# Optimization experiments

Hardware: AMD Instinct MI355X
Metric: run time of the kernel (lower is better)

Reference implementation:

```python
import jax, jax.numpy as jnp
import numpy as np

B, D, K, NDIM = 4, 81, 2048, 4  # batch, feature dim, n mixture components, box coord dims


def setup_inputs() -> dict:
    key = jax.random.key(0)
    k1, k2, k3, k4 = jax.random.split(key, 4)
    x = jax.random.normal(k1, (B, D, K), dtype=jnp.float32)
    # mixture weights, positive and normalized over components
    pi = jax.nn.softmax(jax.random.normal(k2, (B, 1, K), dtype=jnp.float32), axis=2)
    # component means in [0,1] (normalized box coords)
    mu = jax.random.uniform(k3, (B, NDIM, K), dtype=jnp.float32)
    # positive scales
    sig = jax.random.uniform(k4, (B, NDIM, K), dtype=jnp.float32) * 0.1 + 0.01
    return {"x": x, "pi": pi, "mu": mu, "sig": sig}


def _cauchy_pdf(mu, sig, points):
    # mu, sig: (B, 1, NDIM, K); points: (B, P, NDIM, 1)
    d = points - mu
    return sig / (jnp.pi * (d * d + sig * sig))


def reference(x, pi, mu, sig):
    # points = mu.transpose(1,2): evaluate the mixture at each component mean
    points = jnp.transpose(mu, (0, 2, 1))            # (B, K, NDIM)
    comp = _cauchy_pdf(mu[:, None, :, :], sig[:, None, :, :],
                       points[:, :, :, None])        # (B, K, NDIM, K)
    comp = jnp.prod(comp, axis=2)                    # independent dims -> (B, K, K)
    lh = pi * comp                                   # pi (B,1,K) broadcasts over points
    coef = lh / jnp.sum(lh, axis=2, keepdims=True)   # normalize over components
    coef = jax.lax.stop_gradient(coef)               # coef_detach=True
    y = jnp.einsum('bdk,bkm->bdm', x, coef)          # torch.bmm(x, coef)
    return y
```

## Files before the change

kernel.cpp:

```cpp
#include <hip/hip_runtime.h>


typedef float v4f __attribute__((ext_vector_type(4)));
typedef float f32x4 __attribute__((ext_vector_type(4)));
typedef short bf16x8 __attribute__((ext_vector_type(8)));

namespace {
constexpr int BB = 4;
constexpr int DD = 81;
constexpr int KK = 2048;
constexpr int MROWS = 96;
constexpr float INV_PI4 = 1.0f / 97.40909103400243f;

constexpr size_t OFF_XBF = 0;
constexpr size_t OFF_RSP = (size_t)BB * MROWS * KK * 2;
}

__device__ __forceinline__ unsigned short f2bf(float f) {
    union { float f; unsigned int u; } v; v.f = f;
    unsigned int u = v.u;
    unsigned int r = (u + 0x7FFFu + ((u >> 16) & 1u)) >> 16;
    return (unsigned short)r;
}

__global__ __launch_bounds__(256) void rowsum_kernel(const float* __restrict__ pi_,
                                                     const float* __restrict__ mu,
                                                     const float* __restrict__ sig,
                                                     float* __restrict__ rowsumPart) {
    __shared__ v4f   mush[256];
    __shared__ v4f   s2sh[256];
    __shared__ float csh[256];
    __shared__ float red[4][64];

    int blk = blockIdx.x;
    int b   = blk >> 8;
    int pc  = (blk & 255) >> 3;
    int ms  = blk & 7;
    int p0  = pc * 64;
    int m0  = ms * 256;
    int t   = threadIdx.x;
    int lane = t & 63, w = t >> 6;

    const float* mub = mu  + (size_t)b * 4 * KK;
    const float* sgb = sig + (size_t)b * 4 * KK;
    const float* pib = pi_ + (size_t)b * KK;

    {
        int m = m0 + t;
        v4f mm = {mub[m], mub[KK + m], mub[2 * KK + m], mub[3 * KK + m]};
        v4f sg = {sgb[m], sgb[KK + m], sgb[2 * KK + m], sgb[3 * KK + m]};
        mush[t] = mm;
        s2sh[t] = sg * sg;
        csh[t]  = pib[m] * ((sg.x * sg.y) * (sg.z * sg.w)) * INV_PI4;
    }
    int p = p0 + lane;
    v4f mp = {mub[p], mub[KK + p], mub[2 * KK + p], mub[3 * KK + p]};
    __syncthreads();

    float sum = 0.f;
#pragma unroll 4
    for (int i = 0; i < 64; ++i) {
        int mi = w * 64 + i;
        v4f d = mp - mush[mi];
        v4f q = d * d + s2sh[mi];
        float den = (q.x * q.y) * (q.z * q.w);
        sum += csh[mi] * __builtin_amdgcn_rcpf(den);
    }

    red[w][lane] = sum;
    __syncthreads();
    if (t < 64)
        rowsumPart[((size_t)(b * 8 + ms)) * KK + p0 + t] =
            red[0][t] + red[1][t] + red[2][t] + red[3][t];
}

__global__ __launch_bounds__(256) void xbf_kernel(const float* __restrict__ x,
                                                  const float* __restrict__ rowsumPart,
                                                  unsigned short* __restrict__ xbf) {
    int d = blockIdx.x;
    int b = blockIdx.y;
    int t = threadIdx.x;
    unsigned short* orow = xbf + ((size_t)(b * MROWS + d)) * KK;
    const float* xrow = x + ((size_t)(b * DD + d)) * KK;
    const float* rsp  = rowsumPart + (size_t)b * 8 * KK;
#pragma unroll
    for (int j = 0; j < 8; ++j) {
        int p = j * 256 + t;
        float rs = 0.f;
#pragma unroll
        for (int s = 0; s < 8; ++s) rs += rsp[(size_t)s * KK + p];
        float v = 0.f;
        if (d < DD) v = xrow[p] * __builtin_amdgcn_rcpf(rs);
        orow[p] = f2bf(v);
    }
}

__global__ __launch_bounds__(512) void gemm_kernel(const float* __restrict__ pi_,
                                                   const float* __restrict__ mu,
                                                   const float* __restrict__ sig,
                                                   const unsigned short* __restrict__ xbf,
                                                   float* __restrict__ out) {
    __shared__ __align__(16) char smem[49152];
    v4f* mus = (v4f*)smem;
    f32x4 (*red)[6][64] = (f32x4 (*)[6][64])smem;

    int t = threadIdx.x;
    int w = t >> 6, lane = t & 63;
    int r = lane & 15, q = lane >> 4;
    int b  = blockIdx.y;
    int m0 = blockIdx.x * 16;

    const float* mub = mu  + (size_t)b * 4 * KK;
    const float* sgb = sig + (size_t)b * 4 * KK;

    for (int i = t; i < KK; i += 512)
        mus[i] = (v4f){mub[i], mub[KK + i], mub[2 * KK + i], mub[3 * KK + i]};

    int m = m0 + r;
    v4f mm = {mub[m], mub[KK + m], mub[2 * KK + m], mub[3 * KK + m]};
    v4f sg = {sgb[m], sgb[KK + m], sgb[2 * KK + m], sgb[3 * KK + m]};
    v4f s2 = sg * sg;
    float cm = pi_[(size_t)b * KK + m] * ((sg.x * sg.y) * (sg.z * sg.w)) * INV_PI4;

    const unsigned short* Abase = xbf + ((size_t)(b * MROWS + r)) * KK;

    f32x4 acc[6];
#pragma unroll
    for (int i = 0; i < 6; ++i) acc[i] = (f32x4)0.f;

    __syncthreads();

    int pw = w * 256;
#pragma unroll
    for (int ks = 0; ks < 8; ++ks) {
        int pb = pw + ks * 32 + q * 8;
        bf16x8 Bf;
#pragma unroll
        for (int j = 0; j < 8; ++j) {
            v4f mp = mus[pb + j];
            v4f dd = mp - mm;
            v4f qq = dd * dd + s2;
            float den = (qq.x * qq.y) * (qq.z * qq.w);
            float lh = cm * __builtin_amdgcn_rcpf(den);
            Bf[j] = (short)f2bf(lh);
        }
        bf16x8 Af[6];
#pragma unroll
        for (int Mt = 0; Mt < 6; ++Mt)
            Af[Mt] = *(const bf16x8*)(Abase + (size_t)Mt * 16 * KK + pb);
#pragma unroll
        for (int Mt = 0; Mt < 6; ++Mt)
            acc[Mt] = __builtin_amdgcn_mfma_f32_16x16x32_bf16(Af[Mt], Bf, acc[Mt], 0, 0, 0);
    }

    __syncthreads();
#pragma unroll
    for (int Mt = 0; Mt < 6; ++Mt)
        red[w][Mt][lane] = acc[Mt];
    __syncthreads();

    int col = t & 15;
    int dr  = t >> 4;
#pragma unroll
    for (int k = 0; k < 3; ++k) {
        int d = dr + 32 * k;
        if (d < DD) {
            int Mt  = d >> 4;
            int row = d & 15;
            int l   = (row >> 2) * 16 + col;
            int j   = row & 3;
            float s = 0.f;
#pragma unroll
            for (int ww = 0; ww < 8; ++ww) s += red[ww][Mt][l][j];
            out[((size_t)(b * DD + d)) * KK + m0 + col] = s;
        }
    }
}

extern "C" void kernel_launch(void* const* d_in, const int* in_sizes, int n_in,
                              void* d_out, int out_size, void* d_ws, size_t ws_size,
                              hipStream_t stream) {
    const float* x   = (const float*)d_in[0];
    const float* pi_ = (const float*)d_in[1];
    const float* mu  = (const float*)d_in[2];
    const float* sig = (const float*)d_in[3];
    float* out = (float*)d_out;

    unsigned short* xbf = (unsigned short*)((char*)d_ws + OFF_XBF);
    float* rowsumPart   = (float*)((char*)d_ws + OFF_RSP);

    rowsum_kernel<<<1024, 256, 0, stream>>>(pi_, mu, sig, rowsumPart);
    dim3 xg(MROWS, BB);
    xbf_kernel<<<xg, 256, 0, stream>>>(x, rowsumPart, xbf);
    dim3 gg(KK / 16, BB);
    gemm_kernel<<<gg, 512, 0, stream>>>(pi_, mu, sig, xbf, out);
}
```

Measured before the change: 100.2 us.

## Fuse rowsum, scaling and GEMM into one cooperative kernel with grid syncs

```diff
diff --git a/kernel.cpp b/kernel.cpp
--- a/kernel.cpp
+++ b/kernel.cpp
@@ -1,5 +1,8 @@
 #include <hip/hip_runtime.h>
-
+#include <hip/hip_cooperative_groups.h>
+
+
+namespace cg = cooperative_groups;
 
 typedef float v4f __attribute__((ext_vector_type(4)));
 typedef float f32x4 __attribute__((ext_vector_type(4)));
@@ -10,6 +13,8 @@
 constexpr int DD = 81;
 constexpr int KK = 2048;
 constexpr int MROWS = 96;
+constexpr int NBLK = 512;
+constexpr int NTHR = 256;
 constexpr float INV_PI4 = 1.0f / 97.40909103400243f;
 
 constexpr size_t OFF_XBF = 0;
@@ -21,6 +26,161 @@
     unsigned int u = v.u;
     unsigned int r = (u + 0x7FFFu + ((u >> 16) & 1u)) >> 16;
     return (unsigned short)r;
+}
+
+__global__ __launch_bounds__(NTHR, 2) void fused_kernel(const float* __restrict__ x,
+                                                        const float* __restrict__ pi_,
+                                                        const float* __restrict__ mu,
+                                                        const float* __restrict__ sig,
+                                                        unsigned short* __restrict__ xbf,
+                                                        float* __restrict__ rowsumPart,
+                                                        float* __restrict__ out) {
+    __shared__ __align__(16) char smem[32768];
+    cg::grid_group grid = cg::this_grid();
+
+    int g = blockIdx.x;
+    int t = threadIdx.x;
+    int lane = t & 63, w = t >> 6;
+
+    {
+        v4f*   mush = (v4f*)smem;
+        v4f*   s2sh = (v4f*)(smem + 8192);
+        float* csh  = (float*)(smem + 16384);
+        float* red  = (float*)(smem + 18432);
+
+        int b  = g >> 7;
+        int pc = (g & 127) >> 2;
+        int ms = g & 3;
+        int p0 = pc * 64;
+        int m0 = ms * 512;
+
+        const float* mub = mu  + (size_t)b * 4 * KK;
+        const float* sgb = sig + (size_t)b * 4 * KK;
+        const float* pib = pi_ + (size_t)b * KK;
+
+        for (int i = t; i < 512; i += NTHR) {
+            int m = m0 + i;
+            v4f mm = {mub[m], mub[KK + m], mub[2 * KK + m], mub[3 * KK + m]};
+            v4f sg = {sgb[m], sgb[KK + m], sgb[2 * KK + m], sgb[3 * KK + m]};
+            mush[i] = mm;
+            s2sh[i] = sg * sg;
+            csh[i]  = pib[m] * ((sg.x * sg.y) * (sg.z * sg.w)) * INV_PI4;
+        }
+        int p = p0 + lane;
+        v4f mp = {mub[p], mub[KK + p], mub[2 * KK + p], mub[3 * KK + p]};
+        __syncthreads();
+
+        float sum = 0.f;
+#pragma unroll 4
+        for (int i = 0; i < 128; ++i) {
+            int mi = w * 128 + i;
+            v4f d = mp - mush[mi];
+            v4f q = d * d + s2sh[mi];
+            float den = (q.x * q.y) * (q.z * q.w);
+            sum += csh[mi] * __builtin_amdgcn_rcpf(den);
+        }
+
+        red[w * 64 + lane] = sum;
+        __syncthreads();
+        if (t < 64)
+            rowsumPart[((size_t)(b * 4 + ms)) * KK + p0 + t] =
+                red[t] + red[64 + t] + red[128 + t] + red[192 + t];
+    }
+
+    grid.sync();
+
+    {
+        const size_t NE = (size_t)BB * MROWS * KK;
+        size_t tid = (size_t)g * NTHR + t;
+        for (size_t e = tid; e < NE; e += (size_t)NBLK * NTHR) {
+            int p  = (int)(e & (KK - 1));
+            int bd = (int)(e >> 11);
+            int b  = bd / MROWS;
+            int d  = bd - b * MROWS;
+            const float* rsp = rowsumPart + (size_t)b * 4 * KK + p;
+            float rs = rsp[0] + rsp[KK] + rsp[2 * KK] + rsp[3 * KK];
+            float v = 0.f;
+            if (d < DD) v = x[((size_t)(b * DD + d)) * KK + p] * __builtin_amdgcn_rcpf(rs);
+            xbf[e] = f2bf(v);
+        }
+    }
+
+    grid.sync();
+
+    {
+        v4f* mus = (v4f*)smem;
+        f32x4 (*red)[6][64] = (f32x4 (*)[6][64])smem;
+
+        int r = lane & 15, q = lane >> 4;
+        int b  = g >> 7;
+        int m0 = (g & 127) * 16;
+
+        const float* mub = mu  + (size_t)b * 4 * KK;
+        const float* sgb = sig + (size_t)b * 4 * KK;
+
+        __syncthreads();
+        for (int i = t; i < KK; i += NTHR)
+            mus[i] = (v4f){mub[i], mub[KK + i], mub[2 * KK + i], mub[3 * KK + i]};
+
+        int m = m0 + r;
+        v4f mm = {mub[m], mub[KK + m], mub[2 * KK + m], mub[3 * KK + m]};
+        v4f sg = {sgb[m], sgb[KK + m], sgb[2 * KK + m], sgb[3 * KK + m]};
+        v4f s2 = sg * sg;
+        float cm = pi_[(size_t)b * KK + m] * ((sg.x * sg.y) * (sg.z * sg.w)) * INV_PI4;
+
+        const unsigned short* Abase = xbf + ((size_t)(b * MROWS + r)) * KK;
+
+        f32x4 acc[6];
+#pragma unroll
+        for (int i = 0; i < 6; ++i) acc[i] = (f32x4)0.f;
+
+        __syncthreads();
+
+        int pw = w * 512;
+#pragma unroll 4
+        for (int ks = 0; ks < 16; ++ks) {
+            int pb = pw + ks * 32 + q * 8;
+            bf16x8 Bf;
+#pragma unroll
+            for (int j = 0; j < 8; ++j) {
+                v4f mp = mus[pb + j];
+                v4f dd = mp - mm;
+                v4f qq = dd * dd + s2;
+                float den = (qq.x * qq.y) * (qq.z * qq.w);
+                float lh = cm * __builtin_amdgcn_rcpf(den);
+                Bf[j] = (short)f2bf(lh);
+            }
+            bf16x8 Af[6];
+#pragma unroll
+            for (int Mt = 0; Mt < 6; ++Mt)
+                Af[Mt] = *(const bf16x8*)(Abase + (size_t)Mt * 16 * KK + pb);
+#pragma unroll
+            for (int Mt = 0; Mt < 6; ++Mt)
+                acc[Mt] = __builtin_amdgcn_mfma_f32_16x16x32_bf16(Af[Mt], Bf, acc[Mt], 0, 0, 0);
+        }
+
+        __syncthreads();
+#pragma unroll
+        for (int Mt = 0; Mt < 6; ++Mt)
+            red[w][Mt][lane] = acc[Mt];
+        __syncthreads();
+
+        int col = t & 15;
+        int dr  = t >> 4;
+#pragma unroll
+        for (int k = 0; k < 6; ++k) {
+            int d = dr + 16 * k;
+            if (d < DD) {
+                int Mt  = d >> 4;
+                int row = d & 15;
+                int l   = (row >> 2) * 16 + col;
+                int j   = row & 3;
+                float s = red[0][Mt][l][j] + red[1][Mt][l][j] +
+                          red[2][Mt][l][j] + red[3][Mt][l][j];
+                out[((size_t)(b * DD + d)) * KK + m0 + col] = s;
+            }
+        }
+    }
 }
 
 __global__ __launch_bounds__(256) void rowsum_kernel(const float* __restrict__ pi_,
@@ -100,9 +260,9 @@
                                                    const float* __restrict__ sig,
                                                    const unsigned short* __restrict__ xbf,
                                                    float* __restrict__ out) {
-    __shared__ __align__(16) char smem[49152];
-    v4f* mus = (v4f*)smem;
-    f32x4 (*red)[6][64] = (f32x4 (*)[6][64])smem;
+    __shared__ __align__(16) char smem2[49152];
+    v4f* mus = (v4f*)smem2;
+    f32x4 (*red)[6][64] = (f32x4 (*)[6][64])smem2;
 
     int t = threadIdx.x;
     int w = t >> 6, lane = t & 63;
@@ -189,9 +349,15 @@
     unsigned short* xbf = (unsigned short*)((char*)d_ws + OFF_XBF);
     float* rowsumPart   = (float*)((char*)d_ws + OFF_RSP);
 
-    rowsum_kernel<<<1024, 256, 0, stream>>>(pi_, mu, sig, rowsumPart);
-    dim3 xg(MROWS, BB);
-    xbf_kernel<<<xg, 256, 0, stream>>>(x, rowsumPart, xbf);
-    dim3 gg(KK / 16, BB);
-    gemm_kernel<<<gg, 512, 0, stream>>>(pi_, mu, sig, xbf, out);
-}
+    void* args[] = {(void*)&x, (void*)&pi_, (void*)&mu, (void*)&sig,
+                    (void*)&xbf, (void*)&rowsumPart, (void*)&out};
+    hipError_t err = hipLaunchCooperativeKernel((void*)fused_kernel, dim3(NBLK),
+                                                dim3(NTHR), args, 0, stream);
+    if (err != hipSuccess) {
+        rowsum_kernel<<<1024, 256, 0, stream>>>(pi_, mu, sig, rowsumPart);
+        dim3 xg(MROWS, BB);
+        xbf_kernel<<<xg, 256, 0, stream>>>(x, rowsumPart, xbf);
+        dim3 gg(KK / 16, BB);
+        gemm_kernel<<<gg, 512, 0, stream>>>(pi_, mu, sig, xbf, out);
+    }
+}
```

Result: slower. 199.4 us (+99.1%).
